# Optimization experiments

Hardware: AMD Instinct MI355X
Metric: run time of the kernel (lower is better)

Reference implementation:

```python
import jax, jax.numpy as jnp
import numpy as np

EPS = 1e-5
DIL = 1
PAD = 1
STRIDE = 1

def conv2d(x, w, stride=1, pad=1, dil=1):
    return jax.lax.conv_general_dilated(x, w, (stride, stride), [(pad, pad), (pad, pad)],
                                        rhs_dilation=(dil, dil),
                                        dimension_numbers=('NCHW', 'OIHW', 'NCHW'))

def batchnorm(x, g, b, m, v):
    inv = g / jnp.sqrt(v + EPS)
    return x * inv[None, :, None, None] + (b - m * inv)[None, :, None, None]

def _bilinear(img, y, x):
    # img: [C,H,W]; y,x: [Ho,Wo] float sample coords; zero padding outside.
    H, W = img.shape[1], img.shape[2]
    y0 = jnp.floor(y); x0 = jnp.floor(x)
    ty = y - y0; tx = x - x0
    y0i = y0.astype(jnp.int32); x0i = x0.astype(jnp.int32)
    def g(yi, xi):
        valid = (yi >= 0) & (yi < H) & (xi >= 0) & (xi < W)
        v = img[:, jnp.clip(yi, 0, H - 1), jnp.clip(xi, 0, W - 1)]  # [C,Ho,Wo]
        return jnp.where(valid[None], v, jnp.zeros((), img.dtype))
    return (g(y0i, x0i) * ((1 - ty) * (1 - tx))[None]
            + g(y0i, x0i + 1) * ((1 - ty) * tx)[None]
            + g(y0i + 1, x0i) * (ty * (1 - tx))[None]
            + g(y0i + 1, x0i + 1) * (ty * tx)[None])

def deform_conv(x, w, offset, stride=1, pad=1, dil=1):
    # offset: [B, 18, Ho, Wo], channels 0:9 = dy per kernel tap (row-major), 9:18 = dx.
    B, C, H, W = x.shape
    Co = w.shape[0]
    Ho = (H + 2 * pad - dil * 2 - 1) // stride + 1
    Wo = (W + 2 * pad - dil * 2 - 1) // stride + 1
    off = offset.reshape(B, 2, 9, Ho, Wo)
    iy = (jnp.arange(Ho) * stride - pad).astype(x.dtype)
    ix = (jnp.arange(Wo) * stride - pad).astype(x.dtype)
    wk = w.reshape(Co, C, 9)
    out = jnp.zeros((B, Co, Ho, Wo), x.dtype)
    for k in range(9):  # fixed 3x3 kernel taps
        ky, kx = k // 3, k % 3
        ys = iy[:, None] + ky * dil + off[:, 0, k]  # [B,Ho,Wo]
        xs = ix[None, :] + kx * dil + off[:, 1, k]
        val = jax.vmap(_bilinear)(x, ys, xs)        # [B,C,Ho,Wo]
        out = out + jnp.einsum('bchw,oc->bohw', val, wk[:, :, k])
    return out

def offset_bias(dil, dtype):
    bw = jnp.array([[-1., 0., 1.]] * 3, dtype) * (dil - 1)
    bh = bw.T
    return jnp.concatenate([bh.reshape(-1), bw.reshape(-1)])  # [18]

def setup_inputs() -> dict:
    key = jax.random.key(0)
    ks = jax.random.split(key, 12)
    B, C, H, W = 8, 256, 56, 56
    inp = {
        'x': jax.random.normal(ks[0], (B, C, H, W), jnp.float32),
        'conv1_w': jax.random.normal(ks[1], (C, C, 3, 3), jnp.float32) * 0.02,
        'bn1_g': jax.random.normal(ks[2], (C,), jnp.float32) * 0.1 + 1.0,
        'bn1_b': jax.random.normal(ks[3], (C,), jnp.float32) * 0.1,
        'bn1_m': jax.random.normal(ks[4], (C,), jnp.float32) * 0.1,
        'bn1_v': jax.random.uniform(ks[5], (C,), jnp.float32) + 0.5,
        'off_w': jax.random.normal(ks[6], (18, C, 3, 3), jnp.float32) * 0.01,
        'off_b': jnp.zeros((18,), jnp.float32),
        'conv2_w': jax.random.normal(ks[7], (C, C, 3, 3), jnp.float32) * 0.02,
        'bn2_g': jax.random.normal(ks[8], (C,), jnp.float32) * 0.1 + 1.0,
        'bn2_b': jax.random.normal(ks[9], (C,), jnp.float32) * 0.1,
        'bn2_m': jax.random.normal(ks[10], (C,), jnp.float32) * 0.1,
        'bn2_v': jax.random.uniform(ks[11], (C,), jnp.float32) + 0.5,
    }
    return inp

def reference(x, conv1_w, bn1_g, bn1_b, bn1_m, bn1_v, off_w, off_b, conv2_w, bn2_g, bn2_b, bn2_m, bn2_v):
    residual = x
    out = conv2d(x, conv1_w, STRIDE, PAD, DIL)
    out = jax.nn.relu(batchnorm(out, bn1_g, bn1_b, bn1_m, bn1_v))
    offset = conv2d(out, off_w, STRIDE, PAD, DIL) + off_b[None, :, None, None]
    offset = offset + offset_bias(DIL, out.dtype)[None, :, None, None]
    out = deform_conv(out, conv2_w, offset, STRIDE, PAD, DIL)
    out = batchnorm(out, bn2_g, bn2_b, bn2_m, bn2_v)
    return jax.nn.relu(out + residual)
```

## Files before the change

### kernel.cpp

```cpp
#include <hip/hip_runtime.h>

#define NB 8
#define NH 56
#define NW 56
#define NHW 3136
#define NCHW 802816
#define NPIX 25088
#define NHP 58
#define EPSV 1e-5f

typedef float f32x4 __attribute__((ext_vector_type(4)));
typedef __bf16 bf16x8 __attribute__((ext_vector_type(8)));

__device__ __forceinline__ unsigned short f2b(float f) {
  unsigned int u = __float_as_uint(f);
  u += 0x7FFFu + ((u >> 16) & 1u);
  return (unsigned short)(u >> 16);
}
__device__ __forceinline__ float blo(unsigned int u){ return __uint_as_float(u << 16); }
__device__ __forceinline__ float bhi(unsigned int u){ return __uint_as_float(u & 0xFFFF0000u); }
__device__ __forceinline__ unsigned int pack_trunc(float f0, float f1) {
  return __builtin_amdgcn_perm(__float_as_uint(f1), __float_as_uint(f0), 0x07060302u);
}

__global__ __launch_bounds__(256) void prep_x(
    const float* __restrict__ x, unsigned short* __restrict__ xbp)
{
  __shared__ float T[64][65];
  const int pxt  = blockIdx.x * 64;
  const int cg   = blockIdx.y * 64;
  const int b    = pxt / NHW;
  const int rem0 = pxt % NHW;
  const int t    = threadIdx.x;
  const int pl   = t & 63;
  const int c0   = t >> 6;
  const float* src = x + (size_t)b*NCHW + rem0;
  #pragma unroll
  for (int it = 0; it < 16; ++it) {
    int c = c0 + it*4;
    T[c][pl] = src[(size_t)(cg + c)*NHW + pl];
  }
  __syncthreads();
  const int pr = t >> 5;
  const int cp = t & 31;
  #pragma unroll
  for (int it = 0; it < 8; ++it) {
    int pxl = pr + it*8;
    int rem = rem0 + pxl;
    int ho = rem / NW, wo = rem % NW;
    unsigned int pk = ((unsigned int)f2b(T[cp*2+1][pxl]) << 16) | (unsigned int)f2b(T[cp*2][pxl]);
    *(unsigned int*)(xbp + ((size_t)(b*NHP + ho + 1)*NHP + (wo + 1))*256 + cg + cp*2) = pk;
  }
}

__global__ __launch_bounds__(256) void prep_w(
    const float* __restrict__ w, unsigned short* __restrict__ wp)
{
  int i = blockIdx.x*256 + threadIdx.x;
  int co = i / 2304;
  int r  = i % 2304;
  int k  = r >> 8;
  int ci = r & 255;
  wp[i] = f2b(w[((size_t)co*256 + ci)*9 + k]);
}

__global__ __launch_bounds__(256) void prep_w3(
    const float* __restrict__ ow, unsigned short* __restrict__ w3p)
{
  int i = blockIdx.x*256 + threadIdx.x;
  int co = i / 2304;
  int r  = i % 2304;
  int k  = r >> 8;
  int ci = r & 255;
  w3p[i] = (co < 18) ? f2b(ow[((size_t)co*256 + ci)*9 + k]) : (unsigned short)0;
}

__global__ __launch_bounds__(512, 4) void gemm_conv1(
    const unsigned short* __restrict__ xbp, const unsigned short* __restrict__ w1p,
    const float* __restrict__ gam, const float* __restrict__ bet,
    const float* __restrict__ mu,  const float* __restrict__ var,
    unsigned short* __restrict__ t1b)
{
  __shared__ unsigned short SMEM[20480];
  unsigned short* Al = SMEM;
  unsigned short* Bl = SMEM + 4096;

  const int m0   = blockIdx.x * 64;
  const int t    = threadIdx.x;
  const int lane = t & 63;
  const int wv   = t >> 6;
  const int wvM  = wv & 1;
  const int wvN  = wv >> 1;
  const int quad = lane >> 4;
  const int l15  = lane & 15;

  const int srow = t >> 3;
  const int seg  = t & 7;
  {
  }
  const int px  = m0 + srow;
  const int b   = px / NHW, rem = px % NHW;
  const int ho  = rem / NW, wo = rem % NW;
  const unsigned int pbase = ((unsigned int)(b*NHP + ho)*NHP + wo)*256u;

  f32x4 acc[2][4];
  #pragma unroll
  for (int i = 0; i < 2; ++i)
    #pragma unroll
    for (int j = 0; j < 4; ++j) acc[i][j] = (f32x4)(0.f);

  for (int r = 0; r < 36; ++r) {
    const int k = r >> 2, cic = r & 3;
    const int ky = k/3, kx = k - ky*3;
    __syncthreads();
    {
      uint4 q = *(const uint4*)(xbp + pbase + (unsigned int)((ky*NHP + kx)*256 + cic*64 + seg*8));
      *(uint4*)(&Al[srow*64 + ((seg ^ (srow & 7))*8)]) = q;
    }
    #pragma unroll
    for (int u = 0; u < 4; ++u) {
      int tau = t + u*512;
      int row = tau >> 3, sb = tau & 7;
      uint4 q = *(const uint4*)(w1p + (size_t)row*2304 + r*64 + sb*8);
      *(uint4*)(&Bl[row*64 + ((sb ^ (row & 7))*8)]) = q;
    }
    __syncthreads();
    #pragma unroll
    for (int kk = 0; kk < 2; ++kk) {
      const int s8 = (kk*4 + quad) ^ (l15 & 7);
      bf16x8 af[2], bfr[4];
      #pragma unroll
      for (int mt = 0; mt < 2; ++mt)
        af[mt] = *(const bf16x8*)(&Al[(wvM*32 + mt*16 + l15)*64 + s8*8]);
      #pragma unroll
      for (int nt = 0; nt < 4; ++nt)
        bfr[nt] = *(const bf16x8*)(&Bl[(wvN*64 + nt*16 + l15)*64 + s8*8]);
      #pragma unroll
      for (int mt = 0; mt < 2; ++mt)
        #pragma unroll
        for (int nt = 0; nt < 4; ++nt)
          acc[mt][nt] = __builtin_amdgcn_mfma_f32_16x16x32_bf16(af[mt], bfr[nt], acc[mt][nt], 0, 0, 0);
    }
  }

  __syncthreads();
  unsigned short* Sw = SMEM + wv*2304;
  #pragma unroll
  for (int nt = 0; nt < 4; ++nt) {
    const int co = wvN*64 + nt*16 + l15;
    const float inv  = gam[co] * rsqrtf(var[co] + EPSV);
    const float beta = bet[co] - mu[co]*inv;
    #pragma unroll
    for (int mt = 0; mt < 2; ++mt) {
      #pragma unroll
      for (int rr = 0; rr < 4; ++rr) {
        const int pxl = mt*16 + quad*4 + rr;
        float val = acc[mt][nt][rr]*inv + beta;
        val = val > 0.f ? val : 0.f;
        Sw[pxl*72 + nt*16 + l15] = f2b(val);
      }
    }
  }
  #pragma unroll
  for (int i = 0; i < 4; ++i) {
    const int pxl = (lane >> 3) + 8*i;
    const int sc  = lane & 7;
    uint4 q = *(const uint4*)(&Sw[pxl*72 + sc*8]);
    const int pg = m0 + wvM*32 + pxl;
    const int bb = pg / NHW, rm = pg % NHW;
    const int hh = rm / NW, ww = rm % NW;
    *(uint4*)(t1b + ((size_t)(bb*NHP + hh + 1)*NHP + ww + 1)*256 + wvN*64 + sc*8) = q;
  }
}

__global__ __launch_bounds__(256, 4) void gemm_off(
    const unsigned short* __restrict__ t1b, const unsigned short* __restrict__ w3p,
    const float* __restrict__ ob, float* __restrict__ toff)
{
  __shared__ unsigned short Al[4096];
  __shared__ unsigned short Bl[2048];

  const int m0   = blockIdx.x * 64;
  const int t    = threadIdx.x;
  const int lane = t & 63;
  const int wv   = t >> 6;
  const int quad = lane >> 4;
  const int l15  = lane & 15;

  const int arow = t >> 2;
  const int as4  = t & 3;
  const int pxa  = m0 + arow;
  const int ba   = pxa / NHW, rema = pxa % NHW;
  const unsigned int pbase = ((unsigned int)(ba*NHP + rema/NW)*NHP + rema%NW)*256u;

  const int brow = t >> 3;
  const int bs   = t & 7;

  f32x4 acc[2];
  acc[0] = (f32x4)(0.f); acc[1] = (f32x4)(0.f);

  for (int r = 0; r < 36; ++r) {
    const int k = r >> 2, cic = r & 3;
    const int ky = k/3, kx = k - ky*3;
    __syncthreads();
    #pragma unroll
    for (int u = 0; u < 2; ++u) {
      const int sg = as4 + 4*u;
      uint4 q = *(const uint4*)(t1b + pbase + (unsigned int)((ky*NHP + kx)*256 + cic*64 + sg*8));
      *(uint4*)(&Al[arow*64 + ((sg ^ (arow & 7))*8)]) = q;
    }
    {
      uint4 q = *(const uint4*)(w3p + (size_t)brow*2304 + r*64 + bs*8);
      *(uint4*)(&Bl[brow*64 + ((bs ^ (brow & 7))*8)]) = q;
    }
    __syncthreads();
    #pragma unroll
    for (int kk = 0; kk < 2; ++kk) {
      const int s8 = (kk*4 + quad) ^ (l15 & 7);
      bf16x8 af = *(const bf16x8*)(&Al[(wv*16 + l15)*64 + s8*8]);
      #pragma unroll
      for (int nt = 0; nt < 2; ++nt) {
        bf16x8 bfr = *(const bf16x8*)(&Bl[(nt*16 + l15)*64 + s8*8]);
        acc[nt] = __builtin_amdgcn_mfma_f32_16x16x32_bf16(af, bfr, acc[nt], 0, 0, 0);
      }
    }
  }
  #pragma unroll
  for (int nt = 0; nt < 2; ++nt) {
    const int co = nt*16 + l15;
    if (co < 18) {
      const float bias = ob[co];
      #pragma unroll
      for (int rr = 0; rr < 4; ++rr) {
        const int pg = m0 + wv*16 + quad*4 + rr;
        const int bb = pg / NHW, rm = pg % NHW;
        toff[(size_t)bb*(18*NHW) + (size_t)co*NHW + rm] = acc[nt][rr] + bias;
      }
    }
  }
}

__global__ __launch_bounds__(512, 4) void gemm_deform(
    const unsigned short* __restrict__ t1b, const unsigned short* __restrict__ w2p,
    const float* __restrict__ toff, const float* __restrict__ xres,
    const float* __restrict__ gam, const float* __restrict__ bet,
    const float* __restrict__ mu,  const float* __restrict__ var,
    float* __restrict__ outp)
{
  __shared__ unsigned short SMEM[20480];
  unsigned short* Al = SMEM;
  unsigned short* Bl = SMEM + 4096;

  const int m0   = blockIdx.x * 64;
  const int t    = threadIdx.x;
  const int lane = t & 63;
  const int wv   = t >> 6;
  const int wvM  = wv & 1;
  const int wvN  = wv >> 1;
  const int quad = lane >> 4;
  const int l15  = lane & 15;

  const int srow = t >> 3;
  const int seg  = t & 7;
  const int px   = m0 + srow;
  const int b    = px / NHW, rem = px % NHW;
  const int ho   = rem / NW, wo = rem % NW;
  const int obb  = b*(18*NHW) + rem;
  const unsigned int prowb = (unsigned int)(b*NHP);

  f32x4 acc[2][4];
  #pragma unroll
  for (int i = 0; i < 2; ++i)
    #pragma unroll
    for (int j = 0; j < 4; ++j) acc[i][j] = (f32x4)(0.f);

  for (int k = 0; k < 9; ++k) {
    const int ky = k/3, kx = k - ky*3;
    const float offy = toff[obb + k*NHW];
    const float offx = toff[obb + (9+k)*NHW];
    const float yf = (float)(ho - 1 + ky) + offy;
    const float xf = (float)(wo - 1 + kx) + offx;
    const float y0f = floorf(yf), x0f = floorf(xf);
    const float ty = yf - y0f,   tx = xf - x0f;
    const int y0p = (int)y0f + 1, x0p = (int)x0f + 1;
    const int cy0 = min(max(y0p,   0), NHP-1);
    const int cy1 = min(max(y0p+1, 0), NHP-1);
    const int cx0 = min(max(x0p,   0), NHP-1);
    const int cx1 = min(max(x0p+1, 0), NHP-1);
    const float w00 = (1.f-ty)*(1.f-tx);
    const float w01 = (1.f-ty)*tx;
    const float w10 = ty*(1.f-tx);
    const float w11 = ty*tx;
    const unsigned int o00 = ((prowb + cy0)*NHP + cx0)*256u + seg*8u;
    const unsigned int o01 = ((prowb + cy0)*NHP + cx1)*256u + seg*8u;
    const unsigned int o10 = ((prowb + cy1)*NHP + cx0)*256u + seg*8u;
    const unsigned int o11 = ((prowb + cy1)*NHP + cx1)*256u + seg*8u;

    for (int cic = 0; cic < 4; ++cic) {
      const int r = k*4 + cic;
      __syncthreads();
      {
        const unsigned int cio = (unsigned int)(cic*64);
        uint4 q00 = *(const uint4*)(t1b + o00 + cio);
        uint4 q01 = *(const uint4*)(t1b + o01 + cio);
        uint4 q10 = *(const uint4*)(t1b + o10 + cio);
        uint4 q11 = *(const uint4*)(t1b + o11 + cio);
        uint4 res;
        {
          float a0 = w00*blo(q00.x) + w01*blo(q01.x) + w10*blo(q10.x) + w11*blo(q11.x);
          float a1 = w00*bhi(q00.x) + w01*bhi(q01.x) + w10*bhi(q10.x) + w11*bhi(q11.x);
          res.x = pack_trunc(a0, a1);
        }
        {
          float a0 = w00*blo(q00.y) + w01*blo(q01.y) + w10*blo(q10.y) + w11*blo(q11.y);
          float a1 = w00*bhi(q00.y) + w01*bhi(q01.y) + w10*bhi(q10.y) + w11*bhi(q11.y);
          res.y = pack_trunc(a0, a1);
        }
        {
          float a0 = w00*blo(q00.z) + w01*blo(q01.z) + w10*blo(q10.z) + w11*blo(q11.z);
          float a1 = w00*bhi(q00.z) + w01*bhi(q01.z) + w10*bhi(q10.z) + w11*bhi(q11.z);
          res.z = pack_trunc(a0, a1);
        }
        {
          float a0 = w00*blo(q00.w) + w01*blo(q01.w) + w10*blo(q10.w) + w11*blo(q11.w);
          float a1 = w00*bhi(q00.w) + w01*bhi(q01.w) + w10*bhi(q10.w) + w11*bhi(q11.w);
          res.w = pack_trunc(a0, a1);
        }
        *(uint4*)(&Al[srow*64 + ((seg ^ (srow & 7))*8)]) = res;
      }
      #pragma unroll
      for (int u = 0; u < 4; ++u) {
        int tau = t + u*512;
        int row = tau >> 3, sb = tau & 7;
        uint4 q = *(const uint4*)(w2p + (size_t)row*2304 + r*64 + sb*8);
        *(uint4*)(&Bl[row*64 + ((sb ^ (row & 7))*8)]) = q;
      }
      __syncthreads();
      #pragma unroll
      for (int kk = 0; kk < 2; ++kk) {
        const int s8 = (kk*4 + quad) ^ (l15 & 7);
        bf16x8 af[2], bfr[4];
        #pragma unroll
        for (int mt = 0; mt < 2; ++mt)
          af[mt] = *(const bf16x8*)(&Al[(wvM*32 + mt*16 + l15)*64 + s8*8]);
        #pragma unroll
        for (int nt = 0; nt < 4; ++nt)
          bfr[nt] = *(const bf16x8*)(&Bl[(wvN*64 + nt*16 + l15)*64 + s8*8]);
        #pragma unroll
        for (int mt = 0; mt < 2; ++mt)
          #pragma unroll
          for (int nt = 0; nt < 4; ++nt)
            acc[mt][nt] = __builtin_amdgcn_mfma_f32_16x16x32_bf16(af[mt], bfr[nt], acc[mt][nt], 0, 0, 0);
      }
    }
  }

  __syncthreads();
  float* Sl = (float*)SMEM + wv*1056;
  const int pxl_r = lane & 31;
  const int csel  = lane >> 5;
  const int pg    = m0 + wvM*32 + pxl_r;
  const int bo    = pg / NHW, remo = pg % NHW;
  const size_t obase = (size_t)bo*NCHW + remo;
  #pragma unroll
  for (int h = 0; h < 2; ++h) {
    #pragma unroll
    for (int nt2 = 0; nt2 < 2; ++nt2) {
      const int nt = h*2 + nt2;
      #pragma unroll
      for (int mt = 0; mt < 2; ++mt) {
        #pragma unroll
        for (int rr = 0; rr < 4; ++rr) {
          const int pxl = mt*16 + quad*4 + rr;
          Sl[pxl*33 + nt2*16 + l15] = acc[mt][nt][rr];
        }
      }
    }
    #pragma unroll
    for (int j = 0; j < 16; ++j) {
      const int col = csel*16 + j;
      const int co  = wvN*64 + h*32 + col;
      const float inv  = gam[co] * rsqrtf(var[co] + EPSV);
      const float beta = bet[co] - mu[co]*inv;
      const size_t off = obase + (size_t)co*NHW;
      float val = Sl[pxl_r*33 + col];
      float o = val*inv + beta + xres[off];
      outp[off] = o > 0.f ? o : 0.f;
    }
  }
}

extern "C" void kernel_launch(void* const* d_in, const int* in_sizes, int n_in,
                              void* d_out, int out_size, void* d_ws, size_t ws_size,
                              hipStream_t stream) {
  const float* x   = (const float*)d_in[0];
  const float* w1  = (const float*)d_in[1];
  const float* g1  = (const float*)d_in[2];
  const float* b1  = (const float*)d_in[3];
  const float* m1  = (const float*)d_in[4];
  const float* v1  = (const float*)d_in[5];
  const float* ow  = (const float*)d_in[6];
  const float* ob  = (const float*)d_in[7];
  const float* w2  = (const float*)d_in[8];
  const float* g2  = (const float*)d_in[9];
  const float* b2  = (const float*)d_in[10];
  const float* m2  = (const float*)d_in[11];
  const float* v2  = (const float*)d_in[12];
  float* out = (float*)d_out;

  const size_t PADSZ = (size_t)NB*NHP*NHP*256;
  unsigned short* xbp = (unsigned short*)d_ws;
  unsigned short* t1b = xbp + PADSZ;
  float*          tof = (float*)(t1b + PADSZ);
  unsigned short* w1p = (unsigned short*)(tof + (size_t)NB*18*NHW);
  unsigned short* w2p = w1p + (size_t)589824;
  unsigned short* w3p = w2p + (size_t)589824;

  hipMemsetAsync(xbp, 0, 2*PADSZ*sizeof(unsigned short), stream);

  dim3 gp(392, 4, 1);
  prep_x<<<gp, 256, 0, stream>>>(x, xbp);
  prep_w<<<2304, 256, 0, stream>>>(w1, w1p);
  prep_w<<<2304, 256, 0, stream>>>(w2, w2p);
  prep_w3<<<288, 256, 0, stream>>>(ow, w3p);

  gemm_conv1<<<392, 512, 0, stream>>>(xbp, w1p, g1, b1, m1, v1, t1b);
  gemm_off<<<392, 256, 0, stream>>>(t1b, w3p, ob, tof);
  gemm_deform<<<392, 512, 0, stream>>>(t1b, w2p, tof, x, g2, b2, m2, v2, out);
}
```

Before: 263.5 us.

## Prefetch GEMM operands into registers, split-K offset conv, clear only pad borders

All three GEMM kernels now load the next K-slice of A and B into registers while the current slice is computed, and replace the post-store __syncthreads with a barrier that waits only on LDS counters. The offset conv is split four ways along K across blockIdx.y and accumulates with atomics into a pre-zeroed buffer, to raise parallelism for that small GEMM. The full memset of both padded buffers is replaced by a kernel that zeroes only the one-pixel borders. The atomics add contention and nondeterministic summation order, and the prefetch raises register pressure.

```diff
diff --git a/kernel.cpp b/kernel.cpp
--- a/kernel.cpp
+++ b/kernel.cpp
@@ -21,6 +21,26 @@
 __device__ __forceinline__ float bhi(unsigned int u){ return __uint_as_float(u & 0xFFFF0000u); }
 __device__ __forceinline__ unsigned int pack_trunc(float f0, float f1) {
   return __builtin_amdgcn_perm(__float_as_uint(f1), __float_as_uint(f0), 0x07060302u);
+}
+__device__ __forceinline__ void soft_barrier() {
+  __builtin_amdgcn_s_waitcnt(0xC07F);
+  __builtin_amdgcn_s_barrier();
+}
+
+__global__ __launch_bounds__(256) void clear_borders(
+    unsigned short* __restrict__ xbp, unsigned short* __restrict__ t1b)
+{
+  int i = blockIdx.x*256 + threadIdx.x;
+  int q = i & 31; int pid = i >> 5;
+  int b = pid / 228, j = pid % 228;
+  int y, x;
+  if (j < 58)       { y = 0;  x = j; }
+  else if (j < 116) { y = 57; x = j - 58; }
+  else { int jj = j - 116; y = 1 + (jj >> 1); x = (jj & 1) * 57; }
+  size_t addr = ((size_t)(b*NHP + y)*NHP + x)*256 + q*8;
+  uint4 z = make_uint4(0u,0u,0u,0u);
+  *(uint4*)(xbp + addr) = z;
+  *(uint4*)(t1b + addr) = z;
 }
 
 __global__ __launch_bounds__(256) void prep_x(
@@ -96,12 +116,11 @@
 
   const int srow = t >> 3;
   const int seg  = t & 7;
-  {
-  }
+  const int sxor = srow & 7;
   const int px  = m0 + srow;
   const int b   = px / NHW, rem = px % NHW;
   const int ho  = rem / NW, wo = rem % NW;
-  const unsigned int pbase = ((unsigned int)(b*NHP + ho)*NHP + wo)*256u;
+  const unsigned int pbase = ((unsigned int)(b*NHP + ho)*NHP + wo)*256u + seg*8u;
 
   f32x4 acc[2][4];
   #pragma unroll
@@ -109,22 +128,35 @@
     #pragma unroll
     for (int j = 0; j < 4; ++j) acc[i][j] = (f32x4)(0.f);
 
+  uint4 pA, pB0, pB1, pB2, pB3;
+  {
+    pA  = *(const uint4*)(xbp + pbase);
+    const unsigned int rb = seg*8u;
+    pB0 = *(const uint4*)(w1p + (size_t)(srow      )*2304 + rb);
+    pB1 = *(const uint4*)(w1p + (size_t)(srow +  64)*2304 + rb);
+    pB2 = *(const uint4*)(w1p + (size_t)(srow + 128)*2304 + rb);
+    pB3 = *(const uint4*)(w1p + (size_t)(srow + 192)*2304 + rb);
+  }
+
   for (int r = 0; r < 36; ++r) {
-    const int k = r >> 2, cic = r & 3;
-    const int ky = k/3, kx = k - ky*3;
     __syncthreads();
+    *(uint4*)(&Al[srow*64 + ((seg ^ sxor)*8)]) = pA;
+    *(uint4*)(&Bl[(srow      )*64 + ((seg ^ sxor)*8)]) = pB0;
+    *(uint4*)(&Bl[(srow +  64)*64 + ((seg ^ sxor)*8)]) = pB1;
+    *(uint4*)(&Bl[(srow + 128)*64 + ((seg ^ sxor)*8)]) = pB2;
+    *(uint4*)(&Bl[(srow + 192)*64 + ((seg ^ sxor)*8)]) = pB3;
     {
-      uint4 q = *(const uint4*)(xbp + pbase + (unsigned int)((ky*NHP + kx)*256 + cic*64 + seg*8));
-      *(uint4*)(&Al[srow*64 + ((seg ^ (srow & 7))*8)]) = q;
-    }
-    #pragma unroll
-    for (int u = 0; u < 4; ++u) {
-      int tau = t + u*512;
-      int row = tau >> 3, sb = tau & 7;
-      uint4 q = *(const uint4*)(w1p + (size_t)row*2304 + r*64 + sb*8);
-      *(uint4*)(&Bl[row*64 + ((sb ^ (row & 7))*8)]) = q;
-    }
-    __syncthreads();
+      const int rn = (r < 35) ? r + 1 : 35;
+      const int kn = rn >> 2, cicn = rn & 3;
+      const int kyn = kn/3, kxn = kn - kyn*3;
+      pA  = *(const uint4*)(xbp + pbase + (unsigned int)((kyn*NHP + kxn)*256 + cicn*64));
+      const unsigned int rb = (unsigned int)(rn*64) + seg*8u;
+      pB0 = *(const uint4*)(w1p + (size_t)(srow      )*2304 + rb);
+      pB1 = *(const uint4*)(w1p + (size_t)(srow +  64)*2304 + rb);
+      pB2 = *(const uint4*)(w1p + (size_t)(srow + 128)*2304 + rb);
+      pB3 = *(const uint4*)(w1p + (size_t)(srow + 192)*2304 + rb);
+    }
+    soft_barrier();
     #pragma unroll
     for (int kk = 0; kk < 2; ++kk) {
       const int s8 = (kk*4 + quad) ^ (l15 & 7);
@@ -173,14 +205,15 @@
   }
 }
 
-__global__ __launch_bounds__(256, 4) void gemm_off(
+__global__ __launch_bounds__(256, 8) void gemm_off(
     const unsigned short* __restrict__ t1b, const unsigned short* __restrict__ w3p,
     const float* __restrict__ ob, float* __restrict__ toff)
 {
   __shared__ unsigned short Al[4096];
   __shared__ unsigned short Bl[2048];
 
-  const int m0   = blockIdx.x * 64;
+  const int m0 = blockIdx.x * 64;
+  const int kc = blockIdx.y;
   const int t    = threadIdx.x;
   const int lane = t & 63;
   const int wv   = t >> 6;
@@ -189,6 +222,7 @@
 
   const int arow = t >> 2;
   const int as4  = t & 3;
+  const int axor = arow & 7;
   const int pxa  = m0 + arow;
   const int ba   = pxa / NHW, rema = pxa % NHW;
   const unsigned int pbase = ((unsigned int)(ba*NHP + rema/NW)*NHP + rema%NW)*256u;
@@ -197,23 +231,39 @@
   const int bs   = t & 7;
 
   f32x4 acc[2];
-  acc[0] = (f32x4)(0.f); acc[1] = (f32x4)(0.f);
-
-  for (int r = 0; r < 36; ++r) {
-    const int k = r >> 2, cic = r & 3;
+  #pragma unroll
+  for (int nt = 0; nt < 2; ++nt) {
+    float init = 0.f;
+    if (kc == 0) { int co = nt*16 + l15; init = (co < 18) ? ob[co] : 0.f; }
+    acc[nt] = (f32x4)(init);
+  }
+
+  uint4 pA0, pA1, pB;
+  {
+    const int r = kc*9, k = r >> 2, cic = r & 3;
     const int ky = k/3, kx = k - ky*3;
+    const unsigned int base = pbase + (unsigned int)((ky*NHP + kx)*256 + cic*64);
+    pA0 = *(const uint4*)(t1b + base + as4*8);
+    pA1 = *(const uint4*)(t1b + base + (as4+4)*8);
+    pB  = *(const uint4*)(w3p + (size_t)brow*2304 + r*64 + bs*8);
+  }
+
+  for (int rr = 0; rr < 9; ++rr) {
+    const int r = kc*9 + rr;
     __syncthreads();
-    #pragma unroll
-    for (int u = 0; u < 2; ++u) {
-      const int sg = as4 + 4*u;
-      uint4 q = *(const uint4*)(t1b + pbase + (unsigned int)((ky*NHP + kx)*256 + cic*64 + sg*8));
-      *(uint4*)(&Al[arow*64 + ((sg ^ (arow & 7))*8)]) = q;
-    }
+    *(uint4*)(&Al[arow*64 + ((as4     ^ axor)*8)]) = pA0;
+    *(uint4*)(&Al[arow*64 + (((as4+4) ^ axor)*8)]) = pA1;
+    *(uint4*)(&Bl[brow*64 + ((bs ^ (brow & 7))*8)]) = pB;
     {
-      uint4 q = *(const uint4*)(w3p + (size_t)brow*2304 + r*64 + bs*8);
-      *(uint4*)(&Bl[brow*64 + ((bs ^ (brow & 7))*8)]) = q;
-    }
-    __syncthreads();
+      const int rn = (rr < 8) ? r + 1 : r;
+      const int kn = rn >> 2, cicn = rn & 3;
+      const int kyn = kn/3, kxn = kn - kyn*3;
+      const unsigned int base = pbase + (unsigned int)((kyn*NHP + kxn)*256 + cicn*64);
+      pA0 = *(const uint4*)(t1b + base + as4*8);
+      pA1 = *(const uint4*)(t1b + base + (as4+4)*8);
+      pB  = *(const uint4*)(w3p + (size_t)brow*2304 + rn*64 + bs*8);
+    }
+    soft_barrier();
     #pragma unroll
     for (int kk = 0; kk < 2; ++kk) {
       const int s8 = (kk*4 + quad) ^ (l15 & 7);
@@ -229,12 +279,11 @@
   for (int nt = 0; nt < 2; ++nt) {
     const int co = nt*16 + l15;
     if (co < 18) {
-      const float bias = ob[co];
-      #pragma unroll
-      for (int rr = 0; rr < 4; ++rr) {
-        const int pg = m0 + wv*16 + quad*4 + rr;
+      #pragma unroll
+      for (int rr2 = 0; rr2 < 4; ++rr2) {
+        const int pg = m0 + wv*16 + quad*4 + rr2;
         const int bb = pg / NHW, rm = pg % NHW;
-        toff[(size_t)bb*(18*NHW) + (size_t)co*NHW + rm] = acc[nt][rr] + bias;
+        atomicAdd(&toff[(size_t)bb*(18*NHW) + (size_t)co*NHW + rm], acc[nt][rr2]);
       }
     }
   }
@@ -262,6 +311,7 @@
 
   const int srow = t >> 3;
   const int seg  = t & 7;
+  const int sxor = srow & 7;
   const int px   = m0 + srow;
   const int b    = px / NHW, rem = px % NHW;
   const int ho   = rem / NW, wo = rem % NW;
@@ -274,86 +324,106 @@
     #pragma unroll
     for (int j = 0; j < 4; ++j) acc[i][j] = (f32x4)(0.f);
 
-  for (int k = 0; k < 9; ++k) {
-    const int ky = k/3, kx = k - ky*3;
-    const float offy = toff[obb + k*NHW];
-    const float offx = toff[obb + (9+k)*NHW];
-    const float yf = (float)(ho - 1 + ky) + offy;
-    const float xf = (float)(wo - 1 + kx) + offx;
-    const float y0f = floorf(yf), x0f = floorf(xf);
-    const float ty = yf - y0f,   tx = xf - x0f;
-    const int y0p = (int)y0f + 1, x0p = (int)x0f + 1;
-    const int cy0 = min(max(y0p,   0), NHP-1);
-    const int cy1 = min(max(y0p+1, 0), NHP-1);
-    const int cx0 = min(max(x0p,   0), NHP-1);
-    const int cx1 = min(max(x0p+1, 0), NHP-1);
-    const float w00 = (1.f-ty)*(1.f-tx);
-    const float w01 = (1.f-ty)*tx;
-    const float w10 = ty*(1.f-tx);
-    const float w11 = ty*tx;
-    const unsigned int o00 = ((prowb + cy0)*NHP + cx0)*256u + seg*8u;
-    const unsigned int o01 = ((prowb + cy0)*NHP + cx1)*256u + seg*8u;
-    const unsigned int o10 = ((prowb + cy1)*NHP + cx0)*256u + seg*8u;
-    const unsigned int o11 = ((prowb + cy1)*NHP + cx1)*256u + seg*8u;
-
-    for (int cic = 0; cic < 4; ++cic) {
-      const int r = k*4 + cic;
-      __syncthreads();
+  unsigned int o00, o01, o10, o11;
+  float w00, w01, w10, w11;
+#define COORDS(KK) {                                                   \
+    const int ky_ = (KK)/3, kx_ = (KK) - ky_*3;                        \
+    const float offy = toff[obb + (KK)*NHW];                           \
+    const float offx = toff[obb + (9+(KK))*NHW];                       \
+    const float yf = (float)(ho - 1 + ky_) + offy;                     \
+    const float xf = (float)(wo - 1 + kx_) + offx;                     \
+    const float y0f = floorf(yf), x0f = floorf(xf);                    \
+    const float ty = yf - y0f,   tx = xf - x0f;                        \
+    const int y0p = (int)y0f + 1, x0p = (int)x0f + 1;                  \
+    const int cy0 = min(max(y0p,   0), NHP-1);                         \
+    const int cy1 = min(max(y0p+1, 0), NHP-1);                         \
+    const int cx0 = min(max(x0p,   0), NHP-1);                         \
+    const int cx1 = min(max(x0p+1, 0), NHP-1);                         \
+    w00 = (1.f-ty)*(1.f-tx);  w01 = (1.f-ty)*tx;                       \
+    w10 = ty*(1.f-tx);        w11 = ty*tx;                             \
+    o00 = ((prowb + cy0)*NHP + cx0)*256u + seg*8u;                     \
+    o01 = ((prowb + cy0)*NHP + cx1)*256u + seg*8u;                     \
+    o10 = ((prowb + cy1)*NHP + cx0)*256u + seg*8u;                     \
+    o11 = ((prowb + cy1)*NHP + cx1)*256u + seg*8u;                     \
+  }
+
+  COORDS(0);
+  uint4 pc00, pc01, pc10, pc11, pB0, pB1, pB2, pB3;
+  {
+    pc00 = *(const uint4*)(t1b + o00);
+    pc01 = *(const uint4*)(t1b + o01);
+    pc10 = *(const uint4*)(t1b + o10);
+    pc11 = *(const uint4*)(t1b + o11);
+    const unsigned int rb = seg*8u;
+    pB0 = *(const uint4*)(w2p + (size_t)(srow      )*2304 + rb);
+    pB1 = *(const uint4*)(w2p + (size_t)(srow +  64)*2304 + rb);
+    pB2 = *(const uint4*)(w2p + (size_t)(srow + 128)*2304 + rb);
+    pB3 = *(const uint4*)(w2p + (size_t)(srow + 192)*2304 + rb);
+  }
+
+  for (int r = 0; r < 36; ++r) {
+    __syncthreads();
+    {
+      uint4 res;
       {
-        const unsigned int cio = (unsigned int)(cic*64);
-        uint4 q00 = *(const uint4*)(t1b + o00 + cio);
-        uint4 q01 = *(const uint4*)(t1b + o01 + cio);
-        uint4 q10 = *(const uint4*)(t1b + o10 + cio);
-        uint4 q11 = *(const uint4*)(t1b + o11 + cio);
-        uint4 res;
-        {
-          float a0 = w00*blo(q00.x) + w01*blo(q01.x) + w10*blo(q10.x) + w11*blo(q11.x);
-          float a1 = w00*bhi(q00.x) + w01*bhi(q01.x) + w10*bhi(q10.x) + w11*bhi(q11.x);
-          res.x = pack_trunc(a0, a1);
-        }
-        {
-          float a0 = w00*blo(q00.y) + w01*blo(q01.y) + w10*blo(q10.y) + w11*blo(q11.y);
-          float a1 = w00*bhi(q00.y) + w01*bhi(q01.y) + w10*bhi(q10.y) + w11*bhi(q11.y);
-          res.y = pack_trunc(a0, a1);
-        }
-        {
-          float a0 = w00*blo(q00.z) + w01*blo(q01.z) + w10*blo(q10.z) + w11*blo(q11.z);
-          float a1 = w00*bhi(q00.z) + w01*bhi(q01.z) + w10*bhi(q10.z) + w11*bhi(q11.z);
-          res.z = pack_trunc(a0, a1);
-        }
-        {
-          float a0 = w00*blo(q00.w) + w01*blo(q01.w) + w10*blo(q10.w) + w11*blo(q11.w);
-          float a1 = w00*bhi(q00.w) + w01*bhi(q01.w) + w10*bhi(q10.w) + w11*bhi(q11.w);
-          res.w = pack_trunc(a0, a1);
-        }
-        *(uint4*)(&Al[srow*64 + ((seg ^ (srow & 7))*8)]) = res;
-      }
-      #pragma unroll
-      for (int u = 0; u < 4; ++u) {
-        int tau = t + u*512;
-        int row = tau >> 3, sb = tau & 7;
-        uint4 q = *(const uint4*)(w2p + (size_t)row*2304 + r*64 + sb*8);
-        *(uint4*)(&Bl[row*64 + ((sb ^ (row & 7))*8)]) = q;
-      }
-      __syncthreads();
-      #pragma unroll
-      for (int kk = 0; kk < 2; ++kk) {
-        const int s8 = (kk*4 + quad) ^ (l15 & 7);
-        bf16x8 af[2], bfr[4];
-        #pragma unroll
-        for (int mt = 0; mt < 2; ++mt)
-          af[mt] = *(const bf16x8*)(&Al[(wvM*32 + mt*16 + l15)*64 + s8*8]);
+        float a0 = w00*blo(pc00.x) + w01*blo(pc01.x) + w10*blo(pc10.x) + w11*blo(pc11.x);
+        float a1 = w00*bhi(pc00.x) + w01*bhi(pc01.x) + w10*bhi(pc10.x) + w11*bhi(pc11.x);
+        res.x = pack_trunc(a0, a1);
+      }
+      {
+        float a0 = w00*blo(pc00.y) + w01*blo(pc01.y) + w10*blo(pc10.y) + w11*blo(pc11.y);
+        float a1 = w00*bhi(pc00.y) + w01*bhi(pc01.y) + w10*bhi(pc10.y) + w11*bhi(pc11.y);
+        res.y = pack_trunc(a0, a1);
+      }
+      {
+        float a0 = w00*blo(pc00.z) + w01*blo(pc01.z) + w10*blo(pc10.z) + w11*blo(pc11.z);
+        float a1 = w00*bhi(pc00.z) + w01*bhi(pc01.z) + w10*bhi(pc10.z) + w11*bhi(pc11.z);
+        res.z = pack_trunc(a0, a1);
+      }
+      {
+        float a0 = w00*blo(pc00.w) + w01*blo(pc01.w) + w10*blo(pc10.w) + w11*blo(pc11.w);
+        float a1 = w00*bhi(pc00.w) + w01*bhi(pc01.w) + w10*bhi(pc10.w) + w11*bhi(pc11.w);
+        res.w = pack_trunc(a0, a1);
+      }
+      *(uint4*)(&Al[srow*64 + ((seg ^ sxor)*8)]) = res;
+    }
+    *(uint4*)(&Bl[(srow      )*64 + ((seg ^ sxor)*8)]) = pB0;
+    *(uint4*)(&Bl[(srow +  64)*64 + ((seg ^ sxor)*8)]) = pB1;
+    *(uint4*)(&Bl[(srow + 128)*64 + ((seg ^ sxor)*8)]) = pB2;
+    *(uint4*)(&Bl[(srow + 192)*64 + ((seg ^ sxor)*8)]) = pB3;
+    {
+      if ((r & 3) == 3 && r < 35) COORDS((r+1) >> 2);
+      const int rn = (r < 35) ? r + 1 : 35;
+      const unsigned int cio = (unsigned int)((rn & 3)*64);
+      pc00 = *(const uint4*)(t1b + o00 + cio);
+      pc01 = *(const uint4*)(t1b + o01 + cio);
+      pc10 = *(const uint4*)(t1b + o10 + cio);
+      pc11 = *(const uint4*)(t1b + o11 + cio);
+      const unsigned int rb = (unsigned int)(rn*64) + seg*8u;
+      pB0 = *(const uint4*)(w2p + (size_t)(srow      )*2304 + rb);
+      pB1 = *(const uint4*)(w2p + (size_t)(srow +  64)*2304 + rb);
+      pB2 = *(const uint4*)(w2p + (size_t)(srow + 128)*2304 + rb);
+      pB3 = *(const uint4*)(w2p + (size_t)(srow + 192)*2304 + rb);
+    }
+    soft_barrier();
+    #pragma unroll
+    for (int kk = 0; kk < 2; ++kk) {
+      const int s8 = (kk*4 + quad) ^ (l15 & 7);
+      bf16x8 af[2], bfr[4];
+      #pragma unroll
+      for (int mt = 0; mt < 2; ++mt)
+        af[mt] = *(const bf16x8*)(&Al[(wvM*32 + mt*16 + l15)*64 + s8*8]);
+      #pragma unroll
+      for (int nt = 0; nt < 4; ++nt)
+        bfr[nt] = *(const bf16x8*)(&Bl[(wvN*64 + nt*16 + l15)*64 + s8*8]);
+      #pragma unroll
+      for (int mt = 0; mt < 2; ++mt)
         #pragma unroll
         for (int nt = 0; nt < 4; ++nt)
-          bfr[nt] = *(const bf16x8*)(&Bl[(wvN*64 + nt*16 + l15)*64 + s8*8]);
-        #pragma unroll
-        for (int mt = 0; mt < 2; ++mt)
-          #pragma unroll
-          for (int nt = 0; nt < 4; ++nt)
-            acc[mt][nt] = __builtin_amdgcn_mfma_f32_16x16x32_bf16(af[mt], bfr[nt], acc[mt][nt], 0, 0, 0);
-      }
-    }
-  }
+          acc[mt][nt] = __builtin_amdgcn_mfma_f32_16x16x32_bf16(af[mt], bfr[nt], acc[mt][nt], 0, 0, 0);
+    }
+  }
+#undef COORDS
 
   __syncthreads();
   float* Sl = (float*)SMEM + wv*1056;
@@ -416,15 +486,16 @@
   unsigned short* w2p = w1p + (size_t)589824;
   unsigned short* w3p = w2p + (size_t)589824;
 
-  hipMemsetAsync(xbp, 0, 2*PADSZ*sizeof(unsigned short), stream);
-
+  clear_borders<<<228, 256, 0, stream>>>(xbp, t1b);
   dim3 gp(392, 4, 1);
   prep_x<<<gp, 256, 0, stream>>>(x, xbp);
   prep_w<<<2304, 256, 0, stream>>>(w1, w1p);
   prep_w<<<2304, 256, 0, stream>>>(w2, w2p);
   prep_w3<<<288, 256, 0, stream>>>(ow, w3p);
+  hipMemsetAsync(tof, 0, (size_t)NB*18*NHW*sizeof(float), stream);
 
   gemm_conv1<<<392, 512, 0, stream>>>(xbp, w1p, g1, b1, m1, v1, t1b);
-  gemm_off<<<392, 256, 0, stream>>>(t1b, w3p, ob, tof);
+  dim3 go(392, 4, 1);
+  gemm_off<<<go, 256, 0, stream>>>(t1b, w3p, ob, tof);
   gemm_deform<<<392, 512, 0, stream>>>(t1b, w2p, tof, x, g2, b2, m2, v2, out);
 }
```

Result: faster. 255.6 us (-3.0%).
